# Kernel optimization log

Hardware: AMD Instinct MI355X
Metric: run time of the kernel (lower is better)

## Reference

```python
import jax, jax.numpy as jnp
import numpy as np

NUM_HEADS = 16
THETA = 10000.0


def setup_inputs() -> dict:
    key = jax.random.key(0)
    k1, k2, k3, k4 = jax.random.split(key, 4)
    B, T, D = 2, 2048, 1024
    x = jax.random.normal(k1, (B, T, D), dtype=jnp.float32)
    token_positions = jnp.sort(
        jax.random.randint(k2, (B, T), 0, 2048), axis=-1
    ).astype(jnp.int32)
    sigma_qkv = float(np.sqrt(2.0 / (D + 3 * D)))
    sigma_out = float(np.sqrt(2.0 / (D + D)))
    W_qkv = jax.random.normal(k3, (3 * D, D), dtype=jnp.float32) * sigma_qkv
    W_out = jax.random.normal(k4, (D, D), dtype=jnp.float32) * sigma_out
    return {"x": x, "token_positions": token_positions, "W_qkv": W_qkv, "W_out": W_out}


def _apply_rope(t, cos, sin):
    # t: [B, H, T, d_k]; cos/sin: [B, T, d_k//2]
    B, H, T, dk = t.shape
    t2 = t.reshape(B, H, T, dk // 2, 2)
    te, to = t2[..., 0], t2[..., 1]
    c = cos[:, None]  # [B, 1, T, dk//2]
    s = sin[:, None]
    ye = te * c - to * s
    yo = to * c + te * s
    return jnp.stack([ye, yo], axis=-1).reshape(B, H, T, dk)


def reference(x, token_positions, W_qkv, W_out):
    B, T, D = x.shape
    H = NUM_HEADS
    dk = D // H

    # fused QKV projection: [B, T, 3D] -> split (three, h, d) on last dim
    qkv = jnp.einsum("btd,od->bto", x, W_qkv).reshape(B, T, 3, H, dk)
    qkv = jnp.transpose(qkv, (2, 0, 3, 1, 4))  # [3, B, H, T, dk]
    q, k, v = qkv[0], qkv[1], qkv[2]

    # RoPE angles from token positions
    n = jnp.arange(dk // 2, dtype=jnp.float32)
    inv_freq = THETA ** (-2.0 * n / dk)  # [dk//2]
    angles = token_positions.astype(jnp.float32)[..., None] * inv_freq  # [B, T, dk//2]
    cos, sin = jnp.cos(angles), jnp.sin(angles)
    q = _apply_rope(q, cos, sin)
    k = _apply_rope(k, cos, sin)

    # causal scaled dot-product attention
    scores = jnp.einsum("bhid,bhjd->bhij", q, k) / jnp.sqrt(jnp.float32(dk))
    causal = jnp.tril(jnp.ones((T, T), dtype=bool))
    scores = jnp.where(causal, scores, -jnp.inf)
    probs = jax.nn.softmax(scores, axis=-1)
    attn = jnp.einsum("bhij,bhjd->bhid", probs, v)  # [B, H, T, dk]

    concat = jnp.transpose(attn, (0, 2, 1, 3)).reshape(B, T, D)
    return jnp.einsum("btd,od->bto", concat, W_out)
```

## Files before the change

kernel.cpp:

```cpp
#include <hip/hip_runtime.h>
#include <hip/hip_bf16.h>
#include <cmath>

#define T_SEQ 2048
#define D_MODEL 1024
#define NHEAD 16
#define DK 64

typedef short bf16x8 __attribute__((ext_vector_type(8)));
typedef float f32x4 __attribute__((ext_vector_type(4)));
typedef float f32x16 __attribute__((ext_vector_type(16)));
typedef unsigned uint2v __attribute__((ext_vector_type(2)));

union U8 { unsigned u[4]; bf16x8 v; };

#define VMCNT(n) asm volatile("s_waitcnt vmcnt(" #n ")" ::: "memory")
#define BAR() __builtin_amdgcn_s_barrier()
#define SFENCE() __builtin_amdgcn_sched_barrier(0)

__device__ __forceinline__ short f2b(float f) {
    unsigned u = __builtin_bit_cast(unsigned, f);
    unsigned r = (u + 0x7FFFu + ((u >> 16) & 1u)) >> 16;
    return (short)r;
}

__device__ __forceinline__ void gll16(const void* g, void* l) {
    __builtin_amdgcn_global_load_lds(
        (__attribute__((address_space(1))) void*)g,
        (__attribute__((address_space(3))) void*)l, 16, 0, 0);
}

__device__ __forceinline__ bf16x8 lds_frag(const short* base, int row, int chunk) {
    return *reinterpret_cast<const bf16x8*>(
        (const char*)base + row * 128 + ((chunk * 16) ^ ((row & 7) << 4)));
}

__device__ __forceinline__ unsigned pkbf16(float a, float b) {
    unsigned r;
    asm("v_cvt_pk_bf16_f32 %0, %1, %2" : "=v"(r) : "v"(a), "v"(b));
    return r;
}
__device__ __forceinline__ void pl32swap(unsigned& a, unsigned& b) {
    uint2v r = __builtin_amdgcn_permlane32_swap(a, b, false, false);
    a = r.x; b = r.y;
}

__global__ __launch_bounds__(256) void cvt_all(const float* __restrict__ x,
                                               const float* __restrict__ wq,
                                               const float* __restrict__ wo,
                                               const int* __restrict__ pos,
                                               short* __restrict__ xb,
                                               short* __restrict__ wqb,
                                               short* __restrict__ wob,
                                               float* __restrict__ ct,
                                               float* __restrict__ st) {
    int i = blockIdx.x * 256 + threadIdx.x;
    if (i >= 1048576) {
        int j = i - 1048576;
        int bt = j >> 5, n = j & 31;
        float p = (float)pos[bt];
        float invf = expf((float)n * (-2.0f / (float)DK) * 9.210340371976184f);
        float s, c;
        sincosf(p * invf, &s, &c);
        ct[j] = c; st[j] = s;
        return;
    }
    const float* src;
    short* dst;
    int srcoff, c;
    if (i < 524288) {
        c = i;
        int tile = c >> 9, cc = c & 511;
        int kblk = cc >> 7, row = cc & 127;
        int rb = tile >> 5, kb = tile & 31;
        srcoff = (rb * 128 + row) * D_MODEL + kb * 32 + kblk * 8;
        src = x; dst = xb;
    } else if (i < 917504) {
        c = i - 524288;
        int tile = c >> 9, cc = c & 511;
        int kblk = cc >> 7, row = cc & 127;
        int rb = tile >> 5, kb = tile & 31;
        srcoff = (rb * 128 + row) * D_MODEL + kb * 32 + kblk * 8;
        src = wq; dst = wqb;
    } else {
        c = i - 917504;
        int tile = c >> 8, cc = c & 255;
        int kblk = cc >> 6, row = cc & 63;
        int nb = tile >> 5, kb = tile & 31;
        srcoff = (nb * 64 + row) * D_MODEL + kb * 32 + kblk * 8;
        src = wo; dst = wob;
    }
    float4 a = *reinterpret_cast<const float4*>(src + srcoff);
    float4 b = *reinterpret_cast<const float4*>(src + srcoff + 4);
    bf16x8 v;
    v[0] = f2b(a.x); v[1] = f2b(a.y); v[2] = f2b(a.z); v[3] = f2b(a.w);
    v[4] = f2b(b.x); v[5] = f2b(b.y); v[6] = f2b(b.z); v[7] = f2b(b.w);
    reinterpret_cast<bf16x8*>(dst)[c] = v;
}

__global__ __launch_bounds__(256, 3) void gemm_qkv(const short* __restrict__ xb,
                                                   const short* __restrict__ wb,
                                                   const float* __restrict__ ct,
                                                   const float* __restrict__ st,
                                                   short* __restrict__ Qo,
                                                   short* __restrict__ Ko,
                                                   short* __restrict__ Vt) {
    __shared__ short SM[3][8192];
    const int tid = threadIdx.x;
    const int w = tid >> 6, l = tid & 63, lg = l >> 4, li = l & 15;
    const int wr = w >> 1, wc = w & 1;
    const int bn = blockIdx.x * 128, bm = blockIdx.y * 128;

    const short* pA = xb + (size_t)blockIdx.y * 32 * 4096 + (w * 128 + l) * 8;
    const short* pB = wb + (size_t)blockIdx.x * 32 * 4096 + (w * 128 + l) * 8;

    f32x4 zero = {0.f, 0.f, 0.f, 0.f};
    f32x4 acc[4][4];
#pragma unroll
    for (int m = 0; m < 4; ++m)
#pragma unroll
        for (int n = 0; n < 4; ++n) acc[m][n] = zero;

#define GSTAGE(buf, t_)                                               \
    do {                                                              \
        const size_t ko = (size_t)(t_) * 4096;                        \
        gll16(pA + ko,       &SM[buf][w * 1024]);                     \
        gll16(pA + ko + 512, &SM[buf][w * 1024 + 512]);               \
        gll16(pB + ko,       &SM[buf][4096 + w * 1024]);              \
        gll16(pB + ko + 512, &SM[buf][4096 + w * 1024 + 512]);        \
    } while (0)

    GSTAGE(0, 0);
    GSTAGE(1, 1);

    for (int t = 0; t < 32; ++t) {
        if (t < 31) { VMCNT(4); } else { VMCNT(0); }
        BAR();
        SFENCE();
        if (t + 2 < 32) GSTAGE((t + 2) % 3, t + 2);
        const short* Ac = &SM[t % 3][0];
        const short* Bc = &SM[t % 3][4096];
        bf16x8 a[4], b[4];
#pragma unroll
        for (int m = 0; m < 4; ++m)
            a[m] = *reinterpret_cast<const bf16x8*>(&Ac[lg * 1024 + (wr * 64 + m * 16 + li) * 8]);
#pragma unroll
        for (int n = 0; n < 4; ++n)
            b[n] = *reinterpret_cast<const bf16x8*>(&Bc[lg * 1024 + (wc * 64 + n * 16 + li) * 8]);
        __builtin_amdgcn_s_setprio(1);
#pragma unroll
        for (int m = 0; m < 4; ++m)
#pragma unroll
            for (int n = 0; n < 4; ++n)
                acc[m][n] = __builtin_amdgcn_mfma_f32_16x16x32_bf16(a[m], b[n], acc[m][n], 0, 0, 0);
        __builtin_amdgcn_s_setprio(0);
    }
#undef GSTAGE

    const int which = bn >> 10;
    const int h = ((bn >> 6) + wc) & 15;
    if (which == 2) {
        __syncthreads();
        short* scr = &SM[0][0] + w * 4096;
#pragma unroll
        for (int n = 0; n < 4; ++n)
#pragma unroll
            for (int m = 0; m < 4; ++m)
#pragma unroll
                for (int rp = 0; rp < 2; ++rp) {
                    int d = n * 16 + li;
                    int t64 = m * 16 + lg * 4 + rp * 2;
                    unsigned pk = pkbf16(acc[m][n][rp * 2], acc[m][n][rp * 2 + 1]);
                    *reinterpret_cast<unsigned*>(
                        (char*)scr + ((d * 128 + t64 * 2) ^ ((d & 7) << 4))) = pk;
                }
        const int mi0 = bm + wr * 64;
        const int b0 = mi0 >> 11, t0 = mi0 & (T_SEQ - 1);
        const int kvt = t0 >> 6;
        short* vbase = Vt + ((size_t)(b0 * NHEAD + h) * 32 + kvt) * 4096;
        const int ch = l >> 3;
#pragma unroll
        for (int db = 0; db < 8; ++db) {
            int d = db * 8 + (l & 7);
            bf16x8 v = *reinterpret_cast<const bf16x8*>(
                (char*)scr + ((d * 128 + ch * 16) ^ ((d & 7) << 4)));
            *reinterpret_cast<bf16x8*>(vbase + ch * 512 + d * 8) = v;
        }
    } else {
#pragma unroll
        for (int n = 0; n < 4; ++n) {
            const int d = n * 16 + li;
#pragma unroll
            for (int m = 0; m < 4; ++m)
#pragma unroll
                for (int r = 0; r < 4; ++r) {
                    const int mi = bm + wr * 64 + m * 16 + lg * 4 + r;
                    const int b_ = mi >> 11, tt = mi & (T_SEQ - 1);
                    float v = acc[m][n][r];
                    float vp = __shfl_xor(v, 1);
                    int nn = n * 8 + (li >> 1);
                    float c = ct[(size_t)mi * 32 + nn];
                    float s = st[(size_t)mi * 32 + nn];
                    float o = (d & 1) ? (v * c + vp * s) : (v * c - vp * s);
                    if (which == 0) o *= 0.18033688011112042f;
                    short* dst = (which == 0) ? Qo : Ko;
                    dst[((size_t)((b_ * NHEAD + h) * T_SEQ + tt)) * DK + d] = f2b(o);
                }
        }
    }
}

__global__ __launch_bounds__(256, 2) void attn(const short* __restrict__ Q,
                                               const short* __restrict__ K,
                                               const short* __restrict__ Vt,
                                               short* __restrict__ Cc) {
    __shared__ short Kls[3][4096];

    const int bid = blockIdx.x;
    const int ii = bid & 255, rhalf = bid >> 8;
    const int bh = ii & 31;
    const int qt = rhalf ? 15 - (ii >> 5) : (ii >> 5);
    const int ntb = 2 * qt + 2;

    const int tid = threadIdx.x;
    const int w = tid >> 6, l = tid & 63;
    const int l31 = l & 31, hi = l >> 5, hi4 = hi * 4, hi8 = hi * 8;
    const int q0w = qt * 128 + w * 32;
    const int Tw = (q0w + 32 + 63) >> 6;

    const short* Qh = Q + (size_t)bh * T_SEQ * DK;
    const short* Kh = K + (size_t)bh * T_SEQ * DK;
    const short* Vh = Vt + (size_t)bh * 32 * 4096;

    bf16x8 qf[4];
#pragma unroll
    for (int ks = 0; ks < 4; ++ks)
        qf[ks] = *reinterpret_cast<const bf16x8*>(&Qh[(size_t)(q0w + l31) * DK + ks * 16 + hi8]);

    const f32x16 Z16 = {0.f,0.f,0.f,0.f,0.f,0.f,0.f,0.f,0.f,0.f,0.f,0.f,0.f,0.f,0.f,0.f};
    f32x16 o0 = Z16, o1 = Z16;
    float m = -3.0e38f;
    float lsum = 0.f;

    int kr0, kc0, kr1, kc1;
    {
        int c0 = tid;        kr0 = c0 >> 3; kc0 = ((c0 & 7) ^ (kr0 & 7)) * 8;
        int c1 = 256 + tid;  kr1 = c1 >> 3; kc1 = ((c1 & 7) ^ (kr1 & 7)) * 8;
    }
#define KSTAGE(t_)                                                                     \
    do {                                                                               \
        gll16(Kh + (size_t)((t_) * 64 + kr0) * DK + kc0, &Kls[(t_) % 3][w * 512]);     \
        gll16(Kh + (size_t)((t_) * 64 + kr1) * DK + kc1, &Kls[(t_) % 3][2048 + w * 512]); \
    } while (0)

#define VLOAD(dst_, t_)                                                                \
    do {                                                                               \
        const short* vt = Vh + (size_t)(t_) * 4096;                                    \
        dst_[0] = *reinterpret_cast<const bf16x8*>(vt + (0 + hi) * 512 + l31 * 8);     \
        dst_[1] = *reinterpret_cast<const bf16x8*>(vt + (2 + hi) * 512 + l31 * 8);     \
        dst_[2] = *reinterpret_cast<const bf16x8*>(vt + (0 + hi) * 512 + 256 + l31 * 8); \
        dst_[3] = *reinterpret_cast<const bf16x8*>(vt + (2 + hi) * 512 + 256 + l31 * 8); \
        dst_[4] = *reinterpret_cast<const bf16x8*>(vt + (4 + hi) * 512 + l31 * 8);     \
        dst_[5] = *reinterpret_cast<const bf16x8*>(vt + (6 + hi) * 512 + l31 * 8);     \
        dst_[6] = *reinterpret_cast<const bf16x8*>(vt + (4 + hi) * 512 + 256 + l31 * 8); \
        dst_[7] = *reinterpret_cast<const bf16x8*>(vt + (6 + hi) * 512 + 256 + l31 * 8); \
    } while (0)

#define COMPUTE(t_, vv)                                                                \
    do {                                                                               \
        const int n0 = (t_) * 64;                                                      \
        const short* Kc = Kls[(t_) % 3];                                               \
        f32x16 s0 = Z16, s1 = Z16;                                                     \
        __builtin_amdgcn_s_setprio(1);                                                 \
        _Pragma("unroll")                                                              \
        for (int ks = 0; ks < 4; ++ks) {                                               \
            bf16x8 kf0 = lds_frag(Kc, l31,      ks * 2 + hi);                          \
            bf16x8 kf1 = lds_frag(Kc, 32 + l31, ks * 2 + hi);                          \
            s0 = __builtin_amdgcn_mfma_f32_32x32x16_bf16(kf0, qf[ks], s0, 0, 0, 0);    \
            s1 = __builtin_amdgcn_mfma_f32_32x32x16_bf16(kf1, qf[ks], s1, 0, 0, 0);    \
        }                                                                              \
        __builtin_amdgcn_s_setprio(0);                                                 \
        float p[32];                                                                   \
        _Pragma("unroll")                                                              \
        for (int r = 0; r < 16; ++r) { p[r] = s0[r]; p[16 + r] = s1[r]; }              \
        if (n0 + 64 > q0w) {                                                           \
            const int qrel = q0w + l31 - n0;                                           \
            _Pragma("unroll")                                                          \
            for (int r = 0; r < 16; ++r) {                                             \
                const int kvm = (r & 3) + 8 * (r >> 2) + hi4;                          \
                if (kvm > qrel) p[r] = -3.0e38f;                                       \
                if (kvm + 32 > qrel) p[16 + r] = -3.0e38f;                             \
            }                                                                          \
        }                                                                              \
        float t16[16];                                                                 \
        _Pragma("unroll")                                                              \
        for (int r = 0; r < 16; ++r) t16[r] = fmaxf(p[r], p[16 + r]);                  \
        _Pragma("unroll")                                                              \
        for (int d = 8; d >= 1; d >>= 1)                                               \
            _Pragma("unroll")                                                          \
            for (int r = 0; r < 8; ++r)                                                \
                if (r < d) t16[r] = fmaxf(t16[r], t16[r + d]);                         \
        float tmax = fmaxf(t16[0], __shfl_xor(t16[0], 32));                            \
        if (__any(tmax > m + 8.0f)) {                                                  \
            float mnew = fmaxf(m, tmax);                                               \
            float alpha = __builtin_amdgcn_exp2f(m - mnew);                            \
            m = mnew;                                                                  \
            _Pragma("unroll")                                                          \
            for (int r = 0; r < 16; ++r) {                                             \
                float ar = __shfl(alpha, (r & 3) + 8 * (r >> 2) + hi4);                \
                o0[r] *= ar; o1[r] *= ar;                                              \
            }                                                                          \
            lsum *= alpha;                                                             \
        }                                                                              \
        _Pragma("unroll")                                                              \
        for (int r = 0; r < 32; ++r) p[r] = __builtin_amdgcn_exp2f(p[r] - m);          \
        float a16[16];                                                                 \
        _Pragma("unroll")                                                              \
        for (int r = 0; r < 16; ++r) a16[r] = p[r] + p[16 + r];                        \
        _Pragma("unroll")                                                              \
        for (int d = 8; d >= 1; d >>= 1)                                               \
            _Pragma("unroll")                                                          \
            for (int r = 0; r < 8; ++r)                                                \
                if (r < d) a16[r] += a16[r + d];                                       \
        lsum += a16[0] + __shfl_xor(a16[0], 32);                                       \
        __builtin_amdgcn_s_setprio(1);                                                 \
        _Pragma("unroll")                                                              \
        for (int kb = 0; kb < 2; ++kb) {                                               \
            unsigned pk0 = pkbf16(p[kb * 16 + 0],  p[kb * 16 + 1]);                    \
            unsigned pk1 = pkbf16(p[kb * 16 + 2],  p[kb * 16 + 3]);                    \
            unsigned pk2 = pkbf16(p[kb * 16 + 4],  p[kb * 16 + 5]);                    \
            unsigned pk3 = pkbf16(p[kb * 16 + 6],  p[kb * 16 + 7]);                    \
            unsigned pk4 = pkbf16(p[kb * 16 + 8],  p[kb * 16 + 9]);                    \
            unsigned pk5 = pkbf16(p[kb * 16 + 10], p[kb * 16 + 11]);                   \
            unsigned pk6 = pkbf16(p[kb * 16 + 12], p[kb * 16 + 13]);                   \
            unsigned pk7 = pkbf16(p[kb * 16 + 14], p[kb * 16 + 15]);                   \
            pl32swap(pk0, pk2); pl32swap(pk1, pk3);                                    \
            pl32swap(pk4, pk6); pl32swap(pk5, pk7);                                    \
            U8 f0, f1;                                                                 \
            f0.u[0] = pk0; f0.u[1] = pk1; f0.u[2] = pk2; f0.u[3] = pk3;                \
            f1.u[0] = pk4; f1.u[1] = pk5; f1.u[2] = pk6; f1.u[3] = pk7;                \
            o0 = __builtin_amdgcn_mfma_f32_32x32x16_bf16(f0.v, vv[kb * 4 + 0], o0, 0, 0, 0); \
            o0 = __builtin_amdgcn_mfma_f32_32x32x16_bf16(f1.v, vv[kb * 4 + 1], o0, 0, 0, 0); \
            o1 = __builtin_amdgcn_mfma_f32_32x32x16_bf16(f0.v, vv[kb * 4 + 2], o1, 0, 0, 0); \
            o1 = __builtin_amdgcn_mfma_f32_32x32x16_bf16(f1.v, vv[kb * 4 + 3], o1, 0, 0, 0); \
        }                                                                              \
        __builtin_amdgcn_s_setprio(0);                                                 \
    } while (0)

    bf16x8 vA[8], vB[8];

    VLOAD(vA, 0);
    KSTAGE(0);
    KSTAGE(1);

    for (int t = 0; t < ntb; t += 2) {
        VMCNT(2);
        BAR();
        SFENCE();
        VLOAD(vB, t + 1);
        if (t + 2 < ntb) KSTAGE(t + 2);
        if (t < Tw) COMPUTE(t, vA);
        VMCNT(2);
        BAR();
        SFENCE();
        if (t + 2 < ntb) VLOAD(vA, t + 2);
        if (t + 3 < ntb) KSTAGE(t + 3);
        if (t + 1 < Tw) COMPUTE(t + 1, vB);
    }
#undef COMPUTE
#undef VLOAD
#undef KSTAGE

    const int b = bh >> 4, h = bh & 15;
    const float linv = 1.0f / lsum;
#pragma unroll
    for (int r = 0; r < 16; ++r) {
        const int qoff = (r & 3) + 8 * (r >> 2) + hi4;
        float inv = __shfl(linv, qoff);
        const int mg = b * T_SEQ + q0w + qoff;
        const int mb = mg >> 7, row = mg & 127;
        const int kblk = l31 >> 3, el = l & 7;
        Cc[((size_t)(mb * 32 + h * 2 + 0)) * 4096 + kblk * 1024 + row * 8 + el] = f2b(o0[r] * inv);
        Cc[((size_t)(mb * 32 + h * 2 + 1)) * 4096 + kblk * 1024 + row * 8 + el] = f2b(o1[r] * inv);
    }
}

__global__ __launch_bounds__(256, 3) void gemm_out(const short* __restrict__ ab,
                                                   const short* __restrict__ wb,
                                                   float* __restrict__ out) {
    __shared__ short SM[3][6144];
    const int tid = threadIdx.x;
    const int w = tid >> 6, l = tid & 63, lg = l >> 4, li = l & 15;
    const int wr = w >> 1, wc = w & 1;
    const int bn = blockIdx.x * 64, bm = blockIdx.y * 128;

    const short* pA = ab + (size_t)blockIdx.y * 32 * 4096 + (w * 128 + l) * 8;
    const short* pB = wb + (size_t)blockIdx.x * 32 * 2048 + (w * 64 + l) * 8;

    f32x4 zero = {0.f, 0.f, 0.f, 0.f};
    f32x4 acc[4][2];
#pragma unroll
    for (int m = 0; m < 4; ++m)
#pragma unroll
        for (int n = 0; n < 2; ++n) acc[m][n] = zero;

#define OSTAGE(buf, t_)                                                  \
    do {                                                                 \
        gll16(pA + (size_t)(t_) * 4096,       &SM[buf][w * 1024]);       \
        gll16(pA + (size_t)(t_) * 4096 + 512, &SM[buf][w * 1024 + 512]); \
        gll16(pB + (size_t)(t_) * 2048,       &SM[buf][4096 + w * 512]); \
    } while (0)

    OSTAGE(0, 0);
    OSTAGE(1, 1);

    for (int t = 0; t < 32; ++t) {
        if (t < 31) { VMCNT(3); } else { VMCNT(0); }
        BAR();
        SFENCE();
        if (t + 2 < 32) OSTAGE((t + 2) % 3, t + 2);
        const short* Ac = &SM[t % 3][0];
        const short* Bc = &SM[t % 3][4096];
        bf16x8 a[4], b[2];
#pragma unroll
        for (int m = 0; m < 4; ++m)
            a[m] = *reinterpret_cast<const bf16x8*>(&Ac[lg * 1024 + (wr * 64 + m * 16 + li) * 8]);
#pragma unroll
        for (int n = 0; n < 2; ++n)
            b[n] = *reinterpret_cast<const bf16x8*>(&Bc[lg * 512 + (wc * 32 + n * 16 + li) * 8]);
        __builtin_amdgcn_s_setprio(1);
#pragma unroll
        for (int m = 0; m < 4; ++m)
#pragma unroll
            for (int n = 0; n < 2; ++n)
                acc[m][n] = __builtin_amdgcn_mfma_f32_16x16x32_bf16(a[m], b[n], acc[m][n], 0, 0, 0);
        __builtin_amdgcn_s_setprio(0);
    }
#undef OSTAGE

#pragma unroll
    for (int m = 0; m < 4; ++m)
#pragma unroll
        for (int n = 0; n < 2; ++n)
#pragma unroll
            for (int r = 0; r < 4; ++r) {
                const int mi = bm + wr * 64 + m * 16 + lg * 4 + r;
                out[(size_t)mi * D_MODEL + bn + wc * 32 + n * 16 + li] = acc[m][n][r];
            }
}

extern "C" void kernel_launch(void* const* d_in, const int* in_sizes, int n_in,
                              void* d_out, int out_size, void* d_ws, size_t ws_size,
                              hipStream_t stream) {
    const float* x    = (const float*)d_in[0];
    const int*   pos  = (const int*)d_in[1];
    const float* wqkv = (const float*)d_in[2];
    const float* wout = (const float*)d_in[3];
    float* out = (float*)d_out;

    char* ws = (char*)d_ws;
    size_t off = 0;
    short* xb  = (short*)(ws + off); off += (size_t)4096 * 1024 * 2;
    short* wqb = (short*)(ws + off); off += (size_t)3072 * 1024 * 2;
    short* wob = (short*)(ws + off); off += (size_t)1024 * 1024 * 2;
    short* Q   = (short*)(ws + off); off += (size_t)32 * 2048 * 64 * 2;
    short* Kb  = (short*)(ws + off); off += (size_t)32 * 2048 * 64 * 2;
    short* Vt  = (short*)(ws + off); off += (size_t)32 * 32 * 4096 * 2;
    off += 4096;
    short* Cc  = (short*)(ws + off); off += (size_t)4096 * 1024 * 2;
    float* ct  = (float*)(ws + off); off += (size_t)4096 * 32 * 4;
    float* st  = (float*)(ws + off); off += (size_t)4096 * 32 * 4;

    cvt_all<<<4608, 256, 0, stream>>>(x, wqkv, wout, pos, xb, wqb, wob, ct, st);
    gemm_qkv<<<dim3(24, 32), 256, 0, stream>>>(xb, wqb, ct, st, Q, Kb, Vt);
    attn<<<512, 256, 0, stream>>>(Q, Kb, Vt, Cc);
    gemm_out<<<dim3(16, 32), 256, 0, stream>>>(Cc, wob, out);
}
```

Measured before the change: 113.7 us.

## Double-buffer 128-row K phases with one barrier per phase in attention

Replaces the 3-slot, 64-row K ring buffer with two 128-row LDS buffers. Each loop phase now stages K for two tiles at once and needs a single barrier instead of two. V register loads are reissued right after each tile's compute, so they prefetch one phase ahead. This cuts barrier and wait overhead, at the cost of more LDS (32 KB instead of 24 KB) and less lead time for the V loads.

```diff
diff --git a/kernel.cpp b/kernel.cpp
--- a/kernel.cpp
+++ b/kernel.cpp
@@ -214,13 +214,13 @@
                                                const short* __restrict__ K,
                                                const short* __restrict__ Vt,
                                                short* __restrict__ Cc) {
-    __shared__ short Kls[3][4096];
+    __shared__ short Kls[2][8192];
 
     const int bid = blockIdx.x;
     const int ii = bid & 255, rhalf = bid >> 8;
     const int bh = ii & 31;
     const int qt = rhalf ? 15 - (ii >> 5) : (ii >> 5);
-    const int ntb = 2 * qt + 2;
+    const int nph = qt + 1;
 
     const int tid = threadIdx.x;
     const int w = tid >> 6, l = tid & 63;
@@ -247,10 +247,13 @@
         int c0 = tid;        kr0 = c0 >> 3; kc0 = ((c0 & 7) ^ (kr0 & 7)) * 8;
         int c1 = 256 + tid;  kr1 = c1 >> 3; kc1 = ((c1 & 7) ^ (kr1 & 7)) * 8;
     }
-#define KSTAGE(t_)                                                                     \
-    do {                                                                               \
-        gll16(Kh + (size_t)((t_) * 64 + kr0) * DK + kc0, &Kls[(t_) % 3][w * 512]);     \
-        gll16(Kh + (size_t)((t_) * 64 + kr1) * DK + kc1, &Kls[(t_) % 3][2048 + w * 512]); \
+#define KSTAGE(ph)                                                                         \
+    do {                                                                                   \
+        const int b0_ = (ph) * 128;                                                        \
+        gll16(Kh + (size_t)(b0_ + kr0) * DK + kc0,      &Kls[(ph) & 1][w * 512]);          \
+        gll16(Kh + (size_t)(b0_ + kr1) * DK + kc1,      &Kls[(ph) & 1][2048 + w * 512]);   \
+        gll16(Kh + (size_t)(b0_ + 64 + kr0) * DK + kc0, &Kls[(ph) & 1][4096 + w * 512]);   \
+        gll16(Kh + (size_t)(b0_ + 64 + kr1) * DK + kc1, &Kls[(ph) & 1][4096 + 2048 + w * 512]); \
     } while (0)
 
 #define VLOAD(dst_, t_)                                                                \
@@ -269,7 +272,7 @@
 #define COMPUTE(t_, vv)                                                                \
     do {                                                                               \
         const int n0 = (t_) * 64;                                                      \
-        const short* Kc = Kls[(t_) % 3];                                               \
+        const short* Kc = &Kls[((t_) >> 1) & 1][((t_) & 1) * 4096];                    \
         f32x16 s0 = Z16, s1 = Z16;                                                     \
         __builtin_amdgcn_s_setprio(1);                                                 \
         _Pragma("unroll")                                                              \
@@ -349,23 +352,22 @@
 
     bf16x8 vA[8], vB[8];
 
+    KSTAGE(0);
+    SFENCE();
     VLOAD(vA, 0);
-    KSTAGE(0);
-    KSTAGE(1);
-
-    for (int t = 0; t < ntb; t += 2) {
-        VMCNT(2);
+    VLOAD(vB, 1);
+
+    for (int p = 0; p < nph; ++p) {
+        VMCNT(16);
         BAR();
         SFENCE();
-        VLOAD(vB, t + 1);
-        if (t + 2 < ntb) KSTAGE(t + 2);
-        if (t < Tw) COMPUTE(t, vA);
-        VMCNT(2);
-        BAR();
+        if (p + 1 < nph) KSTAGE(p + 1);
         SFENCE();
-        if (t + 2 < ntb) VLOAD(vA, t + 2);
-        if (t + 3 < ntb) KSTAGE(t + 3);
-        if (t + 1 < Tw) COMPUTE(t + 1, vB);
+        const int t0 = 2 * p, t1 = 2 * p + 1;
+        if (t0 < Tw) COMPUTE(t0, vA);
+        if (p + 1 < nph) VLOAD(vA, t0 + 2);
+        if (t1 < Tw) COMPUTE(t1, vB);
+        if (p + 1 < nph) VLOAD(vB, t1 + 2);
     }
 #undef COMPUTE
 #undef VLOAD
```

New measurement: 111.2 us. 1.02x faster.

## Load K fragments directly into registers, dropping LDS staging and barriers

Applied to the files above, without the earlier changes.

The attention kernel no longer stages K tiles through shared memory with global_load_lds and block barriers. Each wave now loads its K fragments straight from global memory into registers, double-buffered together with V, and each wave loops only over its own causal tile count instead of the block-wide count. This removes LDS traffic, barrier synchronisation and wasted iterations for waves that finish early. The cost is that each of the four waves re-reads the same K tile from global/L2 memory, and register pressure rises from the extra K buffers.

```diff
diff --git a/kernel.cpp b/kernel.cpp
--- a/kernel.cpp
+++ b/kernel.cpp
@@ -28,11 +28,6 @@
     __builtin_amdgcn_global_load_lds(
         (__attribute__((address_space(1))) void*)g,
         (__attribute__((address_space(3))) void*)l, 16, 0, 0);
-}
-
-__device__ __forceinline__ bf16x8 lds_frag(const short* base, int row, int chunk) {
-    return *reinterpret_cast<const bf16x8*>(
-        (const char*)base + row * 128 + ((chunk * 16) ^ ((row & 7) << 4)));
 }
 
 __device__ __forceinline__ unsigned pkbf16(float a, float b) {
@@ -214,13 +209,10 @@
                                                const short* __restrict__ K,
                                                const short* __restrict__ Vt,
                                                short* __restrict__ Cc) {
-    __shared__ short Kls[3][4096];
-
     const int bid = blockIdx.x;
     const int ii = bid & 255, rhalf = bid >> 8;
     const int bh = ii & 31;
     const int qt = rhalf ? 15 - (ii >> 5) : (ii >> 5);
-    const int ntb = 2 * qt + 2;
 
     const int tid = threadIdx.x;
     const int w = tid >> 6, l = tid & 63;
@@ -242,42 +234,37 @@
     float m = -3.0e38f;
     float lsum = 0.f;
 
-    int kr0, kc0, kr1, kc1;
-    {
-        int c0 = tid;        kr0 = c0 >> 3; kc0 = ((c0 & 7) ^ (kr0 & 7)) * 8;
-        int c1 = 256 + tid;  kr1 = c1 >> 3; kc1 = ((c1 & 7) ^ (kr1 & 7)) * 8;
-    }
-#define KSTAGE(t_)                                                                     \
+    const short* kp0 = Kh + (size_t)l31 * DK + hi8;
+    const short* kp1 = Kh + (size_t)(32 + l31) * DK + hi8;
+
+#define KVLOAD(kk_, vv_, t_)                                                           \
     do {                                                                               \
-        gll16(Kh + (size_t)((t_) * 64 + kr0) * DK + kc0, &Kls[(t_) % 3][w * 512]);     \
-        gll16(Kh + (size_t)((t_) * 64 + kr1) * DK + kc1, &Kls[(t_) % 3][2048 + w * 512]); \
+        const size_t ko = (size_t)(t_) * 64 * DK;                                      \
+        _Pragma("unroll")                                                              \
+        for (int ks = 0; ks < 4; ++ks) {                                               \
+            kk_[ks]     = *reinterpret_cast<const bf16x8*>(kp0 + ko + ks * 16);        \
+            kk_[4 + ks] = *reinterpret_cast<const bf16x8*>(kp1 + ko + ks * 16);        \
+        }                                                                              \
+        const short* vt = Vh + (size_t)(t_) * 4096;                                    \
+        vv_[0] = *reinterpret_cast<const bf16x8*>(vt + (0 + hi) * 512 + l31 * 8);      \
+        vv_[1] = *reinterpret_cast<const bf16x8*>(vt + (2 + hi) * 512 + l31 * 8);      \
+        vv_[2] = *reinterpret_cast<const bf16x8*>(vt + (0 + hi) * 512 + 256 + l31 * 8); \
+        vv_[3] = *reinterpret_cast<const bf16x8*>(vt + (2 + hi) * 512 + 256 + l31 * 8); \
+        vv_[4] = *reinterpret_cast<const bf16x8*>(vt + (4 + hi) * 512 + l31 * 8);      \
+        vv_[5] = *reinterpret_cast<const bf16x8*>(vt + (6 + hi) * 512 + l31 * 8);      \
+        vv_[6] = *reinterpret_cast<const bf16x8*>(vt + (4 + hi) * 512 + 256 + l31 * 8); \
+        vv_[7] = *reinterpret_cast<const bf16x8*>(vt + (6 + hi) * 512 + 256 + l31 * 8); \
     } while (0)
 
-#define VLOAD(dst_, t_)                                                                \
-    do {                                                                               \
-        const short* vt = Vh + (size_t)(t_) * 4096;                                    \
-        dst_[0] = *reinterpret_cast<const bf16x8*>(vt + (0 + hi) * 512 + l31 * 8);     \
-        dst_[1] = *reinterpret_cast<const bf16x8*>(vt + (2 + hi) * 512 + l31 * 8);     \
-        dst_[2] = *reinterpret_cast<const bf16x8*>(vt + (0 + hi) * 512 + 256 + l31 * 8); \
-        dst_[3] = *reinterpret_cast<const bf16x8*>(vt + (2 + hi) * 512 + 256 + l31 * 8); \
-        dst_[4] = *reinterpret_cast<const bf16x8*>(vt + (4 + hi) * 512 + l31 * 8);     \
-        dst_[5] = *reinterpret_cast<const bf16x8*>(vt + (6 + hi) * 512 + l31 * 8);     \
-        dst_[6] = *reinterpret_cast<const bf16x8*>(vt + (4 + hi) * 512 + 256 + l31 * 8); \
-        dst_[7] = *reinterpret_cast<const bf16x8*>(vt + (6 + hi) * 512 + 256 + l31 * 8); \
-    } while (0)
-
-#define COMPUTE(t_, vv)                                                                \
+#define COMPUTE(t_, kk_, vv_)                                                          \
     do {                                                                               \
         const int n0 = (t_) * 64;                                                      \
-        const short* Kc = Kls[(t_) % 3];                                               \
         f32x16 s0 = Z16, s1 = Z16;                                                     \
         __builtin_amdgcn_s_setprio(1);                                                 \
         _Pragma("unroll")                                                              \
         for (int ks = 0; ks < 4; ++ks) {                                               \
-            bf16x8 kf0 = lds_frag(Kc, l31,      ks * 2 + hi);                          \
-            bf16x8 kf1 = lds_frag(Kc, 32 + l31, ks * 2 + hi);                          \
-            s0 = __builtin_amdgcn_mfma_f32_32x32x16_bf16(kf0, qf[ks], s0, 0, 0, 0);    \
-            s1 = __builtin_amdgcn_mfma_f32_32x32x16_bf16(kf1, qf[ks], s1, 0, 0, 0);    \
+            s0 = __builtin_amdgcn_mfma_f32_32x32x16_bf16(kk_[ks],     qf[ks], s0, 0, 0, 0); \
+            s1 = __builtin_amdgcn_mfma_f32_32x32x16_bf16(kk_[4 + ks], qf[ks], s1, 0, 0, 0); \
         }                                                                              \
         __builtin_amdgcn_s_setprio(0);                                                 \
         float p[32];                                                                   \
@@ -339,37 +326,29 @@
             U8 f0, f1;                                                                 \
             f0.u[0] = pk0; f0.u[1] = pk1; f0.u[2] = pk2; f0.u[3] = pk3;                \
             f1.u[0] = pk4; f1.u[1] = pk5; f1.u[2] = pk6; f1.u[3] = pk7;                \
-            o0 = __builtin_amdgcn_mfma_f32_32x32x16_bf16(f0.v, vv[kb * 4 + 0], o0, 0, 0, 0); \
-            o0 = __builtin_amdgcn_mfma_f32_32x32x16_bf16(f1.v, vv[kb * 4 + 1], o0, 0, 0, 0); \
-            o1 = __builtin_amdgcn_mfma_f32_32x32x16_bf16(f0.v, vv[kb * 4 + 2], o1, 0, 0, 0); \
-            o1 = __builtin_amdgcn_mfma_f32_32x32x16_bf16(f1.v, vv[kb * 4 + 3], o1, 0, 0, 0); \
+            o0 = __builtin_amdgcn_mfma_f32_32x32x16_bf16(f0.v, vv_[kb * 4 + 0], o0, 0, 0, 0); \
+            o0 = __builtin_amdgcn_mfma_f32_32x32x16_bf16(f1.v, vv_[kb * 4 + 1], o0, 0, 0, 0); \
+            o1 = __builtin_amdgcn_mfma_f32_32x32x16_bf16(f0.v, vv_[kb * 4 + 2], o1, 0, 0, 0); \
+            o1 = __builtin_amdgcn_mfma_f32_32x32x16_bf16(f1.v, vv_[kb * 4 + 3], o1, 0, 0, 0); \
         }                                                                              \
         __builtin_amdgcn_s_setprio(0);                                                 \
     } while (0)
 
-    bf16x8 vA[8], vB[8];
-
-    VLOAD(vA, 0);
-    KSTAGE(0);
-    KSTAGE(1);
-
-    for (int t = 0; t < ntb; t += 2) {
-        VMCNT(2);
-        BAR();
-        SFENCE();
-        VLOAD(vB, t + 1);
-        if (t + 2 < ntb) KSTAGE(t + 2);
-        if (t < Tw) COMPUTE(t, vA);
-        VMCNT(2);
-        BAR();
-        SFENCE();
-        if (t + 2 < ntb) VLOAD(vA, t + 2);
-        if (t + 3 < ntb) KSTAGE(t + 3);
-        if (t + 1 < Tw) COMPUTE(t + 1, vB);
+    bf16x8 kA[8], vA[8], kB[8], vB[8];
+
+    KVLOAD(kA, vA, 0);
+    if (1 < Tw) KVLOAD(kB, vB, 1);
+
+    for (int t = 0; t < Tw; t += 2) {
+        COMPUTE(t, kA, vA);
+        if (t + 2 < Tw) KVLOAD(kA, vA, t + 2);
+        if (t + 1 < Tw) {
+            COMPUTE(t + 1, kB, vB);
+            if (t + 3 < Tw) KVLOAD(kB, vB, t + 3);
+        }
     }
 #undef COMPUTE
-#undef VLOAD
-#undef KSTAGE
+#undef KVLOAD
 
     const int b = bh >> 4, h = bh & 15;
     const float linv = 1.0f / lsum;
```

Measured after the change: 113.2 us. No clear change (-0.4%).
